# Kernel optimization log

Measured on AMD Instinct MI355X. Metric: run time of the kernel, lower is better.

The kernel has to match this reference:

```python
import jax, jax.numpy as jnp
from jax import lax
import numpy as np

B, C_IN, H, W = 8, 1024, 64, 64
DI, C_OUT = 512, 1024
BN_EPS = 1e-5


def setup_inputs() -> dict:
    key = jax.random.key(0)
    ks = jax.random.split(key, 5)
    std = 0.01  # torch init.normal_(std=0.01)
    return {
        "x": jax.random.normal(ks[0], (B, C_IN, H, W), jnp.float32),
        "theta_w": jax.random.normal(ks[1], (DI, C_IN), jnp.float32) * std,
        "theta_b": jnp.zeros((DI,), jnp.float32),
        "phi_w": jax.random.normal(ks[2], (DI, C_IN), jnp.float32) * std,
        "phi_b": jnp.zeros((DI,), jnp.float32),
        "g_w": jax.random.normal(ks[3], (DI, C_IN), jnp.float32) * std,
        "g_b": jnp.zeros((DI,), jnp.float32),
        "out_w": jax.random.normal(ks[4], (C_OUT, DI), jnp.float32) * std,
        "out_b": jnp.zeros((C_OUT,), jnp.float32),
        "bn_w": jnp.ones((C_OUT,), jnp.float32),
        "bn_b": jnp.zeros((C_OUT,), jnp.float32),
    }


def _conv1x1(x, w, b):
    # x: [b,c,h,w], w: [o,c] -> [b,o,h,w]
    return jnp.einsum('bchw,oc->bohw', x, w) + b[None, :, None, None]


def reference(x, theta_w, theta_b, phi_w, phi_b, g_w, g_b, out_w, out_b, bn_w, bn_b):
    b, c, h, w = x.shape
    di = theta_w.shape[0]

    theta = _conv1x1(x, theta_w, theta_b).reshape(b, di, h * w)  # [b,di,N]

    # MaxPool2d(kernel=2, stride=2)
    pool = lax.reduce_window(x, -jnp.inf, lax.max,
                             (1, 1, 2, 2), (1, 1, 2, 2), 'VALID')
    phi = _conv1x1(pool, phi_w, phi_b).reshape(b, di, -1)   # [b,di,M]
    g = _conv1x1(pool, g_w, g_b).reshape(b, di, -1)          # [b,di,M]

    # scaled dot-product attention: scores [b,N,M]
    scores = jnp.einsum('bdn,bdm->bnm', theta, phi) * (di ** -0.5)
    p = jax.nn.softmax(scores, axis=-1)

    # t_x = g @ p^T  -> [b,di,N]
    t = jnp.einsum('bdm,bnm->bdn', g, p).reshape(b, di, h, w)

    y = _conv1x1(t, out_w, out_b)  # [b,C_out,h,w]

    # BatchNorm2d (training mode: batch statistics, biased variance)
    mean = jnp.mean(y, axis=(0, 2, 3), keepdims=True)
    var = jnp.var(y, axis=(0, 2, 3), keepdims=True)
    y = (y - mean) * lax.rsqrt(var + BN_EPS)
    y = y * bn_w[None, :, None, None] + bn_b[None, :, None, None]

    return y + x
```

## Files before the change

### kernel.cpp

```cpp
#include <hip/hip_runtime.h>
#include <cstdint>

typedef unsigned short u16;
typedef __attribute__((ext_vector_type(4))) unsigned short u16x4;
typedef __attribute__((ext_vector_type(8))) short short8;
typedef __attribute__((ext_vector_type(4))) float f32x4;

#define DI 512
#define CIN 1024
#define NPIX 4096
#define MPIX 1024

__device__ __forceinline__ float bf2f(u16 u) {
  union { unsigned int i; float f; } v; v.i = ((unsigned int)u) << 16; return v.f;
}
__device__ __forceinline__ u16 f2bf(float f) {
  union { float f; unsigned int i; } v; v.f = f;
  unsigned int r = v.i + 0x7fffu + ((v.i >> 16) & 1u);
  return (u16)(r >> 16);
}
__device__ __forceinline__ void unpack8(uint4 v, float* f) {
  union { unsigned int i; float f; } u;
  u.i = v.x << 16;          f[0] = u.f;
  u.i = v.x & 0xffff0000u;  f[1] = u.f;
  u.i = v.y << 16;          f[2] = u.f;
  u.i = v.y & 0xffff0000u;  f[3] = u.f;
  u.i = v.z << 16;          f[4] = u.f;
  u.i = v.z & 0xffff0000u;  f[5] = u.f;
  u.i = v.w << 16;          f[6] = u.f;
  u.i = v.w & 0xffff0000u;  f[7] = u.f;
}

__device__ __forceinline__ void gload16(const u16* g, u16* l) {
  __builtin_amdgcn_global_load_lds(
      (const __attribute__((address_space(1))) void*)g,
      (__attribute__((address_space(3))) void*)l, 16, 0, 0);
}

__global__ __launch_bounds__(256) void cvt4_kernel(
    const float* __restrict__ s0, const float* __restrict__ s1,
    const float* __restrict__ s2, const float* __restrict__ s3,
    u16* __restrict__ d0, u16* __restrict__ d1,
    u16* __restrict__ d2, u16* __restrict__ d3) {
  int i = blockIdx.x * 256 + threadIdx.x;
  int sel = i >> 17;
  int j = i & 131071;
  const float* src = sel == 0 ? s0 : sel == 1 ? s1 : sel == 2 ? s2 : s3;
  u16* dst = sel == 0 ? d0 : sel == 1 ? d1 : sel == 2 ? d2 : d3;
  float4 v = *(const float4*)(src + (long)j * 4);
  u16x4 w;
  w[0] = f2bf(v.x); w[1] = f2bf(v.y); w[2] = f2bf(v.z); w[3] = f2bf(v.w);
  *(u16x4*)(dst + (long)j * 4) = w;
}

__global__ __launch_bounds__(256) void transpose_kernel(const float* __restrict__ x,
                                                        u16* __restrict__ xT) {
  __shared__ u16 tile[64][72];
  const int b = blockIdx.z;
  const int n0 = blockIdx.x * 64, c0 = blockIdx.y * 64;
  const float* xb = x + (long)b * CIN * NPIX;
  u16* xTb = xT + (long)b * NPIX * CIN;
  const int t = threadIdx.x;
  const int tc = t >> 4, tn = (t & 15) * 4;
  #pragma unroll
  for (int i = 0; i < 4; i++) {
    int c = tc + i * 16;
    float4 v = *(const float4*)(xb + (long)(c0 + c) * NPIX + n0 + tn);
    tile[c][tn + 0] = f2bf(v.x);
    tile[c][tn + 1] = f2bf(v.y);
    tile[c][tn + 2] = f2bf(v.z);
    tile[c][tn + 3] = f2bf(v.w);
  }
  __syncthreads();
  const int tn2 = t >> 4, tc2 = (t & 15) * 4;
  #pragma unroll
  for (int i = 0; i < 4; i++) {
    int n = tn2 + i * 16;
    u16x4 w;
    w[0] = tile[tc2 + 0][n];
    w[1] = tile[tc2 + 1][n];
    w[2] = tile[tc2 + 2][n];
    w[3] = tile[tc2 + 3][n];
    *(u16x4*)(xTb + (long)(n0 + n) * CIN + c0 + tc2) = w;
  }
}

__global__ __launch_bounds__(256) void pool_kernel(const u16* __restrict__ xT,
                                                   u16* __restrict__ poolT) {
  const int idx = blockIdx.x * 256 + threadIdx.x;
  const int cc = (idx & 127) * 8;
  const int m = (idx >> 7) & 1023;
  const int b = idx >> 17;
  const int i = m >> 5, j = m & 31;
  const int n1 = (i * 2) * 64 + j * 2;
  const u16* base = xT + (long)b * NPIX * CIN + cc;
  uint4 v0 = *(const uint4*)(base + (long)(n1) * CIN);
  uint4 v1 = *(const uint4*)(base + (long)(n1 + 1) * CIN);
  uint4 v2 = *(const uint4*)(base + (long)(n1 + 64) * CIN);
  uint4 v3 = *(const uint4*)(base + (long)(n1 + 65) * CIN);
  float f0[8], f1[8], f2[8], f3[8];
  unpack8(v0, f0); unpack8(v1, f1); unpack8(v2, f2); unpack8(v3, f3);
  u16 r[8] __attribute__((aligned(16)));
  #pragma unroll
  for (int k = 0; k < 8; k++) {
    float mx = fmaxf(fmaxf(f0[k], f1[k]), fmaxf(f2[k], f3[k]));
    r[k] = f2bf(mx);
  }
  *(uint4*)(poolT + ((long)b * MPIX + m) * CIN + cc) = *(uint4*)r;
}

template<int OM, bool HAS_BIAS, bool HAS_CS, bool HAS_SHIFT, bool HAS_EXP, bool HAS_PSUM2>
__global__ __launch_bounds__(256)
void gemm_tn(const u16* __restrict__ A, const u16* __restrict__ B,
             void* __restrict__ Cv,
             const float* __restrict__ bias, long sBias,
             const float* __restrict__ cs, long sCS,
             const float* __restrict__ shift, long sShift,
             float* __restrict__ psum_out,
             float scale, int M, int N, int K, long sA, long sB, long sC)
{
  A += blockIdx.z * sA;
  B += blockIdx.z * sB;
  if (HAS_BIAS) bias += blockIdx.z * sBias;
  if (HAS_CS) cs += blockIdx.z * sCS;
  if (HAS_SHIFT) shift += blockIdx.z * sShift;
  const int bm = blockIdx.y * 128;
  const int bn = blockIdx.x * 128;
  __shared__ __align__(16) u16 smem[128 * 128];
  u16* As = smem;
  u16* Bs = smem + 128 * 64;
  __shared__ float psum[4][128];
  const int tid = threadIdx.x;
  const int lane = tid & 63;
  const int wave = tid >> 6;
  const int wm = (wave >> 1) * 64;
  const int wn = (wave & 1) * 64;
  const int lr = lane & 15;
  const int q  = lane >> 4;
  const int sxor = lane & 7;
  f32x4 acc[4][4] = {};

  const int swz = ((lane & 7) ^ (lane >> 3)) * 8;
  const long grow = 32 * wave + (lane >> 3);
  const u16* Ag = A + ((long)bm + grow) * K + swz;
  const u16* Bg = B + ((long)bn + grow) * K + swz;

  for (int kt = 0; kt < K; kt += 64) {
    __syncthreads();
    #pragma unroll
    for (int i = 0; i < 4; i++) {
      gload16(Ag + (long)(8 * i) * K + kt, &As[(wave * 4 + i) * 512]);
      gload16(Bg + (long)(8 * i) * K + kt, &Bs[(wave * 4 + i) * 512]);
    }
    __syncthreads();
    #pragma unroll
    for (int kk = 0; kk < 2; kk++) {
      short8 av[4], bv[4];
      #pragma unroll
      for (int mi = 0; mi < 4; mi++)
        av[mi] = *(const short8*)&As[(wm + mi * 16 + lr) * 64 +
                                     (((kk << 2) + q) ^ sxor) * 8];
      #pragma unroll
      for (int ni = 0; ni < 4; ni++)
        bv[ni] = *(const short8*)&Bs[(wn + ni * 16 + lr) * 64 +
                                     (((kk << 2) + q) ^ sxor) * 8];
      #pragma unroll
      for (int mi = 0; mi < 4; mi++) {
        #pragma unroll
        for (int ni = 0; ni < 4; ni++)
          acc[mi][ni] = __builtin_amdgcn_mfma_f32_16x16x32_bf16(
              av[mi], bv[ni], acc[mi][ni], 0, 0, 0);
      }
    }
  }

  __syncthreads();
  const int dr = (lane >> 4) * 4;
  float rowsum[4][4];
  float rowsq[4][4];
  if (HAS_EXP || HAS_PSUM2) {
    #pragma unroll
    for (int mi = 0; mi < 4; mi++)
      #pragma unroll
      for (int r = 0; r < 4; r++) { rowsum[mi][r] = 0.f; rowsq[mi][r] = 0.f; }
  }
  #pragma unroll
  for (int mi = 0; mi < 4; mi++) {
    const int rowl = wm + mi * 16 + dr;
    const int rowb = bm + rowl;
    float bvs[4] = {0.f, 0.f, 0.f, 0.f};
    float shv[4] = {0.f, 0.f, 0.f, 0.f};
    if (HAS_BIAS) {
      #pragma unroll
      for (int r = 0; r < 4; r++) bvs[r] = bias[rowb + r];
    }
    if (HAS_SHIFT) {
      #pragma unroll
      for (int r = 0; r < 4; r++) shv[r] = shift[rowb + r];
    }
    #pragma unroll
    for (int ni = 0; ni < 4; ni++) {
      const int coll = wn + ni * 16 + lr;
      const float csv = HAS_CS ? cs[bn + coll] : 1.0f;
      float v[4];
      #pragma unroll
      for (int r = 0; r < 4; r++) {
        float t = acc[mi][ni][r] * scale;
        if (HAS_CS) t *= csv;
        if (HAS_SHIFT) t -= shv[r];
        if (HAS_BIAS) t += bvs[r];
        if (HAS_EXP) t = expf(t);
        if (HAS_EXP || HAS_PSUM2) rowsum[mi][r] += t;
        if (HAS_PSUM2) rowsq[mi][r] += t * t;
        v[r] = t;
      }
      if (OM == 1) {
        u16x4 w;
        #pragma unroll
        for (int r = 0; r < 4; r++) w[r] = f2bf(v[r]);
        unsigned bo = (unsigned)((coll * 128 + rowl) * 2) ^ ((coll & 7) << 4);
        *(u16x4*)((char*)smem + bo) = w;
      } else {
        #pragma unroll
        for (int r = 0; r < 4; r++) smem[(rowl + r) * 128 + coll] = f2bf(v[r]);
      }
    }
  }
  if (HAS_EXP || HAS_PSUM2) {
    #pragma unroll
    for (int msk = 1; msk < 16; msk <<= 1)
      #pragma unroll
      for (int mi = 0; mi < 4; mi++)
        #pragma unroll
        for (int r = 0; r < 4; r++) {
          rowsum[mi][r] += __shfl_xor(rowsum[mi][r], msk);
          if (HAS_PSUM2) rowsq[mi][r] += __shfl_xor(rowsq[mi][r], msk);
        }
    if ((lane & 15) == 0) {
      #pragma unroll
      for (int mi = 0; mi < 4; mi++)
        #pragma unroll
        for (int r = 0; r < 4; r++) {
          psum[wave & 1][wm + mi * 16 + dr + r] = rowsum[mi][r];
          if (HAS_PSUM2) psum[2 + (wave & 1)][wm + mi * 16 + dr + r] = rowsq[mi][r];
        }
    }
  }
  __syncthreads();
  u16* C = (u16*)Cv + blockIdx.z * sC;
  if (OM == 1) {
    #pragma unroll
    for (int i = 0; i < 8; i++) {
      const int chunk = i * 256 + tid;
      const int coll = chunk >> 4, rq = chunk & 15;
      unsigned bo = (unsigned)(coll * 256 + rq * 16) ^ ((coll & 7) << 4);
      uint4 w = *(const uint4*)((const char*)smem + bo);
      *(uint4*)(C + (long)(bn + coll) * M + bm + rq * 8) = w;
    }
  } else {
    #pragma unroll
    for (int i = 0; i < 8; i++) {
      const int chunk = i * 256 + tid;
      const int row = chunk >> 4, cq = chunk & 15;
      uint4 w = *(const uint4*)(smem + row * 128 + cq * 8);
      *(uint4*)(C + (long)(bm + row) * N + bn + cq * 8) = w;
    }
  }
  if (HAS_EXP || HAS_PSUM2) {
    if (tid < 128) {
      if (HAS_EXP)
        psum_out[((long)blockIdx.z * gridDim.x + blockIdx.x) * 4096 + bm + tid] =
            psum[0][tid] + psum[1][tid];
      if (HAS_PSUM2) {
        const long blk = ((long)blockIdx.z * gridDim.y + blockIdx.y) * gridDim.x
                         + blockIdx.x;
        psum_out[blk * 256 + tid] = psum[0][tid] + psum[1][tid];
        psum_out[blk * 256 + 128 + tid] = psum[2][tid] + psum[3][tid];
      }
    }
  }
}

__global__ __launch_bounds__(256) void inv_kernel(const float* __restrict__ partial,
                                                  float* __restrict__ inv) {
  const int idx = blockIdx.x * 256 + threadIdx.x;
  const int b = idx >> 12, n = idx & 4095;
  const float* p = partial + (long)b * 32768 + n;
  float s = 0.f;
  #pragma unroll
  for (int x = 0; x < 8; x++) s += p[(long)x * 4096];
  inv[idx] = 1.0f / s;
}

__global__ __launch_bounds__(256) void gbar_kernel(const u16* __restrict__ g_n,
                                                   float* __restrict__ gbar) {
  const int row = blockIdx.x * 4 + (threadIdx.x >> 6);
  const int lane = threadIdx.x & 63;
  const long base = (long)row * MPIX + lane * 16;
  uint4 va = *(const uint4*)(g_n + base);
  uint4 vb = *(const uint4*)(g_n + base + 8);
  float f[16];
  unpack8(va, f); unpack8(vb, f + 8);
  float s = 0.f;
  #pragma unroll
  for (int j = 0; j < 16; j++) s += f[j];
  #pragma unroll
  for (int off = 32; off > 0; off >>= 1) s += __shfl_xor(s, off);
  if (lane == 0) gbar[row] = s * (1.0f / 1024.0f);
}

__global__ __launch_bounds__(256) void c0_kernel(const float* __restrict__ out_w,
                                                 const float* __restrict__ out_b,
                                                 const float* __restrict__ gbar,
                                                 float* __restrict__ c0) {
  const int idx = blockIdx.x * 4 + (threadIdx.x >> 6);
  const int lane = threadIdx.x & 63;
  const int b = idx >> 10, c = idx & 1023;
  const int d0 = lane * 8;
  float4 w0 = *(const float4*)(out_w + (long)c * DI + d0);
  float4 w1 = *(const float4*)(out_w + (long)c * DI + d0 + 4);
  float4 g0 = *(const float4*)(gbar + (long)b * DI + d0);
  float4 g1 = *(const float4*)(gbar + (long)b * DI + d0 + 4);
  float s = w0.x * g0.x + w0.y * g0.y + w0.z * g0.z + w0.w * g0.w
          + w1.x * g1.x + w1.y * g1.y + w1.z * g1.z + w1.w * g1.w;
  #pragma unroll
  for (int off = 32; off > 0; off >>= 1) s += __shfl_xor(s, off);
  if (lane == 0) c0[idx] = out_b[c] + s;
}

__global__ __launch_bounds__(256) void stats2_kernel(const float* __restrict__ partial,
                                                     const float* __restrict__ c0,
                                                     float* __restrict__ stats) {
  const int co = blockIdx.x * 256 + threadIdx.x;
  const int by = co >> 7, r = co & 127;
  float sd = 0.f, sd2 = 0.f, sbc = 0.f;
  for (int b = 0; b < 8; b++) {
    float sb = 0.f, qb = 0.f;
    #pragma unroll
    for (int bx = 0; bx < 32; bx++) {
      const long blk = (((long)b * 8 + by) * 32 + bx) * 256;
      sb += partial[blk + r];
      qb += partial[blk + 128 + r];
    }
    sd += sb; sd2 += qb;
    sbc += c0[b * 1024 + co] * sb;
  }
  float sc0 = 0.f, sc02 = 0.f;
  #pragma unroll
  for (int b = 0; b < 8; b++) {
    float c = c0[b * 1024 + co];
    sc0 += c; sc02 += c * c;
  }
  stats[co] = 4096.0f * sc0 + sd;
  stats[1024 + co] = 4096.0f * sc02 + 2.0f * sbc + sd2;
}

__global__ __launch_bounds__(256) void final_kernel(const u16* __restrict__ dy,
    const float* __restrict__ x, const float* __restrict__ stats,
    const float* __restrict__ c0,
    const float* __restrict__ bnw, const float* __restrict__ bnb,
    float* __restrict__ out) {
  const int bc = blockIdx.x;
  const int co = bc & 1023;
  const float mean = stats[co] * (1.0f / 32768.0f);
  const float var = stats[1024 + co] * (1.0f / 32768.0f) - mean * mean;
  const float inv = rsqrtf(var + 1e-5f) * bnw[co];
  const float addc = bnb[co] - mean * inv + c0[bc] * inv;
  const long base = (long)bc * 4096;
  const int t = threadIdx.x;
  #pragma unroll
  for (int i = 0; i < 2; i++) {
    const long off = base + (long)(i * 256 + t) * 8;
    uint4 v = *(const uint4*)(dy + off);
    float f[8]; unpack8(v, f);
    const float4 x0 = *(const float4*)(x + off);
    const float4 x1 = *(const float4*)(x + off + 4);
    float4 o0, o1;
    o0.x = f[0] * inv + addc + x0.x;
    o0.y = f[1] * inv + addc + x0.y;
    o0.z = f[2] * inv + addc + x0.z;
    o0.w = f[3] * inv + addc + x0.w;
    o1.x = f[4] * inv + addc + x1.x;
    o1.y = f[5] * inv + addc + x1.y;
    o1.z = f[6] * inv + addc + x1.z;
    o1.w = f[7] * inv + addc + x1.w;
    *(float4*)(out + off) = o0;
    *(float4*)(out + off + 4) = o1;
  }
}

extern "C" void kernel_launch(void* const* d_in, const int* in_sizes, int n_in,
                              void* d_out, int out_size, void* d_ws, size_t ws_size,
                              hipStream_t stream) {
  (void)in_sizes; (void)n_in; (void)out_size; (void)ws_size;
  const float* x       = (const float*)d_in[0];
  const float* theta_w = (const float*)d_in[1];
  const float* theta_b = (const float*)d_in[2];
  const float* phi_w   = (const float*)d_in[3];
  const float* phi_b   = (const float*)d_in[4];
  const float* g_w     = (const float*)d_in[5];
  const float* g_b     = (const float*)d_in[6];
  const float* out_w   = (const float*)d_in[7];
  const float* out_b   = (const float*)d_in[8];
  const float* bn_w    = (const float*)d_in[9];
  const float* bn_b    = (const float*)d_in[10];
  float* out = (float*)d_out;
  char* ws = (char*)d_ws;
  const size_t MB = 1024 * 1024;

  u16* xT     = (u16*)(ws + 0 * MB);
  u16* poolT  = (u16*)(ws + 64 * MB);
  u16* w_th   = (u16*)(ws + 80 * MB);
  u16* w_ph   = (u16*)(ws + 81 * MB);
  u16* w_g    = (u16*)(ws + 82 * MB);
  u16* thetaT = (u16*)(ws + 84 * MB);
  u16* phiT   = (u16*)(ws + 116 * MB);
  u16* g_n    = (u16*)(ws + 124 * MB);
  u16* e      = (u16*)(ws + 132 * MB);
  u16* tT     = (u16*)(ws + 196 * MB);
  u16* w_out  = (u16*)(ws + 228 * MB);
  float* inv_s = (float*)(ws + 229 * MB);
  float* gbar  = (float*)(ws + 229 * MB + 131072);
  float* c0b   = (float*)(ws + 229 * MB + 147456);
  float* stats = (float*)(ws + 229 * MB + 180224);
  float* partial = (float*)(ws + 230 * MB);
  float* partial2 = (float*)(ws + 231 * MB);
  u16* dy = xT;

  cvt4_kernel<<<2048, 256, 0, stream>>>(theta_w, phi_w, g_w, out_w,
                                        w_th, w_ph, w_g, w_out);
  transpose_kernel<<<dim3(64, 16, 8), 256, 0, stream>>>(x, xT);
  pool_kernel<<<4096, 256, 0, stream>>>(xT, poolT);
  gemm_tn<1, true, false, false, false, false><<<dim3(32, 4, 8), 256, 0, stream>>>(
      w_th, xT, thetaT, theta_b, 0L, nullptr, 0L, nullptr, 0L, nullptr,
      1.0f, 512, 4096, 1024, 0L, (long)NPIX * CIN, (long)NPIX * DI);
  gemm_tn<1, true, false, false, false, false><<<dim3(8, 4, 8), 256, 0, stream>>>(
      w_ph, poolT, phiT, phi_b, 0L, nullptr, 0L, nullptr, 0L, nullptr,
      1.0f, 512, 1024, 1024, 0L, (long)MPIX * CIN, (long)MPIX * DI);
  gemm_tn<0, true, false, false, false, false><<<dim3(8, 4, 8), 256, 0, stream>>>(
      w_g, poolT, g_n, g_b, 0L, nullptr, 0L, nullptr, 0L, nullptr,
      1.0f, 512, 1024, 1024, 0L, (long)MPIX * CIN, (long)DI * MPIX);
  gbar_kernel<<<1024, 256, 0, stream>>>(g_n, gbar);
  c0_kernel<<<2048, 256, 0, stream>>>(out_w, out_b, gbar, c0b);
  gemm_tn<0, false, false, false, true, false><<<dim3(8, 32, 8), 256, 0, stream>>>(
      thetaT, phiT, e, nullptr, 0L, nullptr, 0L, nullptr, 0L, partial,
      0.044194173824159216f, 4096, 1024, 512,
      (long)NPIX * DI, (long)MPIX * DI, (long)NPIX * MPIX);
  inv_kernel<<<128, 256, 0, stream>>>(partial, inv_s);
  gemm_tn<1, false, true, true, false, false><<<dim3(32, 4, 8), 256, 0, stream>>>(
      g_n, e, tT, nullptr, 0L, inv_s, 4096L, gbar, 512L, nullptr,
      1.0f, 512, 4096, 1024,
      (long)DI * MPIX, (long)NPIX * MPIX, (long)NPIX * DI);
  gemm_tn<0, false, false, false, false, true><<<dim3(32, 8, 8), 256, 0, stream>>>(
      w_out, tT, dy, nullptr, 0L, nullptr, 0L, nullptr, 0L, partial2,
      1.0f, 1024, 4096, 512, 0L, (long)NPIX * DI, (long)1024 * NPIX);
  stats2_kernel<<<4, 256, 0, stream>>>(partial2, c0b, stats);
  final_kernel<<<8192, 256, 0, stream>>>(dy, x, stats, c0b, bn_w, bn_b, out);
}
```

Before: 384.3 us.

## Fuse phi and g projections into one GEMM, fold softmax normalizer into PV GEMM

The phi and g 1x1 convolutions share the pooled input, so they now run as one GEMM with M=1024. Tiles in the upper half write g in row-major layout with a separate bias and emit per-row partial sums, so gbar comes from a tiny reduction instead of a pass over g. The inv_kernel launch is removed: the PV GEMM sums the softmax partials and takes the reciprocal itself for its column tile. This saves two kernel launches and one re-read of g, at the cost of a more branchy epilogue and redundant reciprocal work across blocks.

Measured after the change: 365.2 us. 1.05x faster.

```diff
diff --git a/kernel.cpp b/kernel.cpp
--- a/kernel.cpp
+++ b/kernel.cpp
@@ -109,11 +109,13 @@
   *(uint4*)(poolT + ((long)b * MPIX + m) * CIN + cc) = *(uint4*)r;
 }
 
-template<int OM, bool HAS_BIAS, bool HAS_CS, bool HAS_SHIFT, bool HAS_EXP, bool HAS_PSUM2>
+template<int OM, bool HAS_BIAS, bool HAS_CS, bool HAS_SHIFT, bool HAS_EXP,
+         bool HAS_PSUM2, bool HAS_CSP>
 __global__ __launch_bounds__(256)
 void gemm_tn(const u16* __restrict__ A, const u16* __restrict__ B,
-             void* __restrict__ Cv,
-             const float* __restrict__ bias, long sBias,
+             void* __restrict__ Cv, void* __restrict__ Cv2,
+             const float* __restrict__ bias, const float* __restrict__ bias2,
+             long sBias,
              const float* __restrict__ cs, long sCS,
              const float* __restrict__ shift, long sShift,
              float* __restrict__ psum_out,
@@ -122,7 +124,7 @@
   A += blockIdx.z * sA;
   B += blockIdx.z * sB;
   if (HAS_BIAS) bias += blockIdx.z * sBias;
-  if (HAS_CS) cs += blockIdx.z * sCS;
+  if (HAS_CS || HAS_CSP) cs += blockIdx.z * sCS;
   if (HAS_SHIFT) shift += blockIdx.z * sShift;
   const int bm = blockIdx.y * 128;
   const int bn = blockIdx.x * 128;
@@ -138,7 +140,17 @@
   const int lr = lane & 15;
   const int q  = lane >> 4;
   const int sxor = lane & 7;
+  const bool gps = (OM == 3) && (bm >= 512);
   f32x4 acc[4][4] = {};
+
+  if (HAS_CSP) {
+    if (tid < 128) {
+      float s = 0.f;
+      #pragma unroll
+      for (int xx = 0; xx < 8; xx++) s += cs[xx * 4096 + bn + tid];
+      psum[0][tid] = 1.0f / s;
+    }
+  }
 
   const int swz = ((lane & 7) ^ (lane >> 3)) * 8;
   const long grow = 32 * wave + (lane >> 3);
@@ -174,16 +186,23 @@
     }
   }
 
+  float invc[4];
+  if (HAS_CSP) {
+    #pragma unroll
+    for (int ni = 0; ni < 4; ni++) invc[ni] = psum[0][wn + ni * 16 + lr];
+  }
   __syncthreads();
   const int dr = (lane >> 4) * 4;
+  const bool trans_out = (OM == 1) || (OM == 3 && !gps);
   float rowsum[4][4];
   float rowsq[4][4];
-  if (HAS_EXP || HAS_PSUM2) {
+  if (HAS_EXP || HAS_PSUM2 || gps) {
     #pragma unroll
     for (int mi = 0; mi < 4; mi++)
       #pragma unroll
       for (int r = 0; r < 4; r++) { rowsum[mi][r] = 0.f; rowsq[mi][r] = 0.f; }
   }
+  const float* bp = (OM == 3 && gps) ? bias2 - 512 : bias;
   #pragma unroll
   for (int mi = 0; mi < 4; mi++) {
     const int rowl = wm + mi * 16 + dr;
@@ -192,7 +211,7 @@
     float shv[4] = {0.f, 0.f, 0.f, 0.f};
     if (HAS_BIAS) {
       #pragma unroll
-      for (int r = 0; r < 4; r++) bvs[r] = bias[rowb + r];
+      for (int r = 0; r < 4; r++) bvs[r] = bp[rowb + r];
     }
     if (HAS_SHIFT) {
       #pragma unroll
@@ -201,20 +220,20 @@
     #pragma unroll
     for (int ni = 0; ni < 4; ni++) {
       const int coll = wn + ni * 16 + lr;
-      const float csv = HAS_CS ? cs[bn + coll] : 1.0f;
+      const float csv = HAS_CSP ? invc[ni] : (HAS_CS ? cs[bn + coll] : 1.0f);
       float v[4];
       #pragma unroll
       for (int r = 0; r < 4; r++) {
         float t = acc[mi][ni][r] * scale;
-        if (HAS_CS) t *= csv;
+        if (HAS_CS || HAS_CSP) t *= csv;
         if (HAS_SHIFT) t -= shv[r];
         if (HAS_BIAS) t += bvs[r];
         if (HAS_EXP) t = expf(t);
-        if (HAS_EXP || HAS_PSUM2) rowsum[mi][r] += t;
+        if (HAS_EXP || HAS_PSUM2 || gps) rowsum[mi][r] += t;
         if (HAS_PSUM2) rowsq[mi][r] += t * t;
         v[r] = t;
       }
-      if (OM == 1) {
+      if (trans_out) {
         u16x4 w;
         #pragma unroll
         for (int r = 0; r < 4; r++) w[r] = f2bf(v[r]);
@@ -226,7 +245,7 @@
       }
     }
   }
-  if (HAS_EXP || HAS_PSUM2) {
+  if (HAS_EXP || HAS_PSUM2 || gps) {
     #pragma unroll
     for (int msk = 1; msk < 16; msk <<= 1)
       #pragma unroll
@@ -247,26 +266,29 @@
     }
   }
   __syncthreads();
-  u16* C = (u16*)Cv + blockIdx.z * sC;
-  if (OM == 1) {
+  if (trans_out) {
+    const int Ms = (OM == 3) ? 512 : M;
+    u16* C = (u16*)Cv + blockIdx.z * sC;
     #pragma unroll
     for (int i = 0; i < 8; i++) {
       const int chunk = i * 256 + tid;
       const int coll = chunk >> 4, rq = chunk & 15;
       unsigned bo = (unsigned)(coll * 256 + rq * 16) ^ ((coll & 7) << 4);
       uint4 w = *(const uint4*)((const char*)smem + bo);
-      *(uint4*)(C + (long)(bn + coll) * M + bm + rq * 8) = w;
+      *(uint4*)(C + (long)(bn + coll) * Ms + bm + rq * 8) = w;
     }
   } else {
+    u16* C = (OM == 3) ? (u16*)Cv2 + blockIdx.z * sC : (u16*)Cv + blockIdx.z * sC;
+    const int rbase = (OM == 3) ? bm - 512 : bm;
     #pragma unroll
     for (int i = 0; i < 8; i++) {
       const int chunk = i * 256 + tid;
       const int row = chunk >> 4, cq = chunk & 15;
       uint4 w = *(const uint4*)(smem + row * 128 + cq * 8);
-      *(uint4*)(C + (long)(bm + row) * N + bn + cq * 8) = w;
-    }
-  }
-  if (HAS_EXP || HAS_PSUM2) {
+      *(uint4*)(C + (long)(rbase + row) * N + bn + cq * 8) = w;
+    }
+  }
+  if (HAS_EXP || HAS_PSUM2 || gps) {
     if (tid < 128) {
       if (HAS_EXP)
         psum_out[((long)blockIdx.z * gridDim.x + blockIdx.x) * 4096 + bm + tid] =
@@ -277,36 +299,22 @@
         psum_out[blk * 256 + tid] = psum[0][tid] + psum[1][tid];
         psum_out[blk * 256 + 128 + tid] = psum[2][tid] + psum[3][tid];
       }
-    }
-  }
-}
-
-__global__ __launch_bounds__(256) void inv_kernel(const float* __restrict__ partial,
-                                                  float* __restrict__ inv) {
+      if (gps)
+        psum_out[((long)blockIdx.z * gridDim.x + blockIdx.x) * 512 +
+                 (bm - 512) + tid] = psum[0][tid] + psum[1][tid];
+    }
+  }
+}
+
+__global__ __launch_bounds__(256) void gbar_kernel(const float* __restrict__ g_ps,
+                                                   float* __restrict__ gbar) {
   const int idx = blockIdx.x * 256 + threadIdx.x;
-  const int b = idx >> 12, n = idx & 4095;
-  const float* p = partial + (long)b * 32768 + n;
+  const int b = idx >> 9, d = idx & 511;
+  const float* p = g_ps + (long)b * 8 * 512 + d;
   float s = 0.f;
   #pragma unroll
-  for (int x = 0; x < 8; x++) s += p[(long)x * 4096];
-  inv[idx] = 1.0f / s;
-}
-
-__global__ __launch_bounds__(256) void gbar_kernel(const u16* __restrict__ g_n,
-                                                   float* __restrict__ gbar) {
-  const int row = blockIdx.x * 4 + (threadIdx.x >> 6);
-  const int lane = threadIdx.x & 63;
-  const long base = (long)row * MPIX + lane * 16;
-  uint4 va = *(const uint4*)(g_n + base);
-  uint4 vb = *(const uint4*)(g_n + base + 8);
-  float f[16];
-  unpack8(va, f); unpack8(vb, f + 8);
-  float s = 0.f;
-  #pragma unroll
-  for (int j = 0; j < 16; j++) s += f[j];
-  #pragma unroll
-  for (int off = 32; off > 0; off >>= 1) s += __shfl_xor(s, off);
-  if (lane == 0) gbar[row] = s * (1.0f / 1024.0f);
+  for (int xx = 0; xx < 8; xx++) s += p[(long)xx * 512];
+  gbar[idx] = s * (1.0f / 1024.0f);
 }
 
 __global__ __launch_bounds__(256) void c0_kernel(const float* __restrict__ out_w,
@@ -419,41 +427,42 @@
   u16* e      = (u16*)(ws + 132 * MB);
   u16* tT     = (u16*)(ws + 196 * MB);
   u16* w_out  = (u16*)(ws + 228 * MB);
-  float* inv_s = (float*)(ws + 229 * MB);
-  float* gbar  = (float*)(ws + 229 * MB + 131072);
-  float* c0b   = (float*)(ws + 229 * MB + 147456);
-  float* stats = (float*)(ws + 229 * MB + 180224);
+  float* gbar  = (float*)(ws + 229 * MB);
+  float* c0b   = (float*)(ws + 229 * MB + 16384);
+  float* stats = (float*)(ws + 229 * MB + 49152);
   float* partial = (float*)(ws + 230 * MB);
   float* partial2 = (float*)(ws + 231 * MB);
+  float* g_ps = (float*)(ws + 233 * MB);
   u16* dy = xT;
 
   cvt4_kernel<<<2048, 256, 0, stream>>>(theta_w, phi_w, g_w, out_w,
                                         w_th, w_ph, w_g, w_out);
   transpose_kernel<<<dim3(64, 16, 8), 256, 0, stream>>>(x, xT);
   pool_kernel<<<4096, 256, 0, stream>>>(xT, poolT);
-  gemm_tn<1, true, false, false, false, false><<<dim3(32, 4, 8), 256, 0, stream>>>(
-      w_th, xT, thetaT, theta_b, 0L, nullptr, 0L, nullptr, 0L, nullptr,
-      1.0f, 512, 4096, 1024, 0L, (long)NPIX * CIN, (long)NPIX * DI);
-  gemm_tn<1, true, false, false, false, false><<<dim3(8, 4, 8), 256, 0, stream>>>(
-      w_ph, poolT, phiT, phi_b, 0L, nullptr, 0L, nullptr, 0L, nullptr,
-      1.0f, 512, 1024, 1024, 0L, (long)MPIX * CIN, (long)MPIX * DI);
-  gemm_tn<0, true, false, false, false, false><<<dim3(8, 4, 8), 256, 0, stream>>>(
-      w_g, poolT, g_n, g_b, 0L, nullptr, 0L, nullptr, 0L, nullptr,
-      1.0f, 512, 1024, 1024, 0L, (long)MPIX * CIN, (long)DI * MPIX);
-  gbar_kernel<<<1024, 256, 0, stream>>>(g_n, gbar);
+  gemm_tn<1, true, false, false, false, false, false>
+      <<<dim3(32, 4, 8), 256, 0, stream>>>(
+      w_th, xT, thetaT, nullptr, theta_b, nullptr, 0L, nullptr, 0L, nullptr, 0L,
+      nullptr, 1.0f, 512, 4096, 1024, 0L, (long)NPIX * CIN, (long)NPIX * DI);
+  gemm_tn<3, true, false, false, false, false, false>
+      <<<dim3(8, 8, 8), 256, 0, stream>>>(
+      w_ph, poolT, phiT, g_n, phi_b, g_b, 0L, nullptr, 0L, nullptr, 0L,
+      g_ps, 1.0f, 1024, 1024, 1024, 0L, (long)MPIX * CIN, (long)MPIX * DI);
+  gbar_kernel<<<16, 256, 0, stream>>>(g_ps, gbar);
   c0_kernel<<<2048, 256, 0, stream>>>(out_w, out_b, gbar, c0b);
-  gemm_tn<0, false, false, false, true, false><<<dim3(8, 32, 8), 256, 0, stream>>>(
-      thetaT, phiT, e, nullptr, 0L, nullptr, 0L, nullptr, 0L, partial,
-      0.044194173824159216f, 4096, 1024, 512,
+  gemm_tn<0, false, false, false, true, false, false>
+      <<<dim3(8, 32, 8), 256, 0, stream>>>(
+      thetaT, phiT, e, nullptr, nullptr, nullptr, 0L, nullptr, 0L, nullptr, 0L,
+      partial, 0.044194173824159216f, 4096, 1024, 512,
       (long)NPIX * DI, (long)MPIX * DI, (long)NPIX * MPIX);
-  inv_kernel<<<128, 256, 0, stream>>>(partial, inv_s);
-  gemm_tn<1, false, true, true, false, false><<<dim3(32, 4, 8), 256, 0, stream>>>(
-      g_n, e, tT, nullptr, 0L, inv_s, 4096L, gbar, 512L, nullptr,
-      1.0f, 512, 4096, 1024,
+  gemm_tn<1, false, false, true, false, false, true>
+      <<<dim3(32, 4, 8), 256, 0, stream>>>(
+      g_n, e, tT, nullptr, nullptr, nullptr, 0L, partial, 32768L, gbar, 512L,
+      nullptr, 1.0f, 512, 4096, 1024,
       (long)DI * MPIX, (long)NPIX * MPIX, (long)NPIX * DI);
-  gemm_tn<0, false, false, false, false, true><<<dim3(32, 8, 8), 256, 0, stream>>>(
-      w_out, tT, dy, nullptr, 0L, nullptr, 0L, nullptr, 0L, partial2,
-      1.0f, 1024, 4096, 512, 0L, (long)NPIX * DI, (long)1024 * NPIX);
+  gemm_tn<0, false, false, false, false, true, false>
+      <<<dim3(32, 8, 8), 256, 0, stream>>>(
+      w_out, tT, dy, nullptr, nullptr, nullptr, 0L, nullptr, 0L, nullptr, 0L,
+      partial2, 1.0f, 1024, 4096, 512, 0L, (long)NPIX * DI, (long)1024 * NPIX);
   stats2_kernel<<<4, 256, 0, stream>>>(partial2, c0b, stats);
   final_kernel<<<8192, 256, 0, stream>>>(dy, x, stats, c0b, bn_w, bn_b, out);
 }
```
